# Performance work log

Measured on AMD Instinct MI355X. Metric: run time of the kernel, lower is better.

## Reference

```python
import jax, jax.numpy as jnp
import numpy as np

N, F, H, O = 3072, 128, 16, 8  # nodes, in_channels, hidden_channels, out_channels


def setup_inputs() -> dict:
    key = jax.random.key(0)
    ks = jax.random.split(key, 8)
    s = 0.01  # xavier gain=0.01 in original init -> small weights
    return {
        "x": jax.random.normal(ks[0], (N, F), dtype=jnp.float32),
        "edge_index": jax.random.randint(ks[1], (2, N * 32), 0, N, dtype=jnp.int64),
        "node_distances": jax.random.uniform(ks[2], (N, N), dtype=jnp.float32),
        "normalization_matrix": jnp.ones((N, N), dtype=jnp.float32),
        # per-feature MLPs fs[f]: Linear(1,H) -> ReLU -> (Dropout p=0) -> Linear(H,O), stacked over F
        "W1": s * jax.random.normal(ks[3], (F, H), dtype=jnp.float32),
        "b1": jnp.zeros((F, H), dtype=jnp.float32),
        "W2": s * jax.random.normal(ks[4], (F, H, O), dtype=jnp.float32),
        "b2": jnp.zeros((F, O), dtype=jnp.float32),
        # rho MLP: Linear(1,H) -> ReLU -> Linear(H,O) (bias=True since is_graph_task=False)
        "rW1": s * jax.random.normal(ks[5], (H,), dtype=jnp.float32),
        "rb1": jnp.zeros((H,), dtype=jnp.float32),
        "rW2": s * jax.random.normal(ks[6], (H, O), dtype=jnp.float32),
        "rb2": jnp.zeros((O,), dtype=jnp.float32),
    }


def reference(x, edge_index, node_distances, normalization_matrix,
              W1, b1, W2, b2, rW1, rb1, rW2, rb2):
    # --- per-feature tiny MLPs, vectorized over the feature axis ---
    # h[n,f,:] = relu(x[n,f] * W1[f] + b1[f])
    h = jax.nn.relu(x[:, :, None] * W1[None, :, :] + b1[None, :, :])  # [N,F,H]
    fx = jnp.einsum('nfh,fho->nfo', h, W2) + b2[None, :, :]           # [N,F,O]
    # sum over features first (commutes with the matmul's F-reduction)
    g = fx.sum(axis=1)                                                 # [N,O]

    # --- rho MLP on normalized pairwise distances ---
    d = node_distances / normalization_matrix                          # [N,N]
    hd = jax.nn.relu(d[:, :, None] * rW1 + rb1)                        # [N,N,H]
    m = jnp.einsum('nmh,ho->nmo', hd, rW2) + rb2                       # [N,N,O]

    # out.T in torch: mf = m_dist_perm @ fx_perm summed over features -> [N,O]
    out = jnp.einsum('nmo,mo->no', m, g)                               # [N,O]
    return out
```

## Files before the change

kernel.cpp:

```cpp
#include <hip/hip_runtime.h>
#include <hip/hip_bf16.h>
#include <math.h>

#define NN 3072
#define FF 128
#define HH 16
#define OO 8

#define MC   1024
#define NCH  3
#define RPB  8

#define OFF_GT   0

#define NPB 4

__global__ __launch_bounds__(128) void gnan_g_kernel(
    const float* __restrict__ x,
    const float* __restrict__ W1,
    const float* __restrict__ b1,
    const float* __restrict__ W2,
    const float* __restrict__ b2,
    float* __restrict__ gT,
    float* __restrict__ out)
{
    const int f  = threadIdx.x;
    const int n0 = blockIdx.x * NPB;

    {
        const int gid = blockIdx.x * 128 + threadIdx.x;
        if (gid < NN * OO / 4)
            reinterpret_cast<float4*>(out)[gid] = make_float4(0.f, 0.f, 0.f, 0.f);
    }

    float xv[NPB];
#pragma unroll
    for (int ni = 0; ni < NPB; ++ni)
        xv[ni] = x[(size_t)(n0 + ni) * FF + f];

    const float4 b2a = *reinterpret_cast<const float4*>(b2 + f * OO);
    const float4 b2b = *reinterpret_cast<const float4*>(b2 + f * OO + 4);

    float acc[NPB][OO];
#pragma unroll
    for (int ni = 0; ni < NPB; ++ni) {
        acc[ni][0] = b2a.x; acc[ni][1] = b2a.y; acc[ni][2] = b2a.z; acc[ni][3] = b2a.w;
        acc[ni][4] = b2b.x; acc[ni][5] = b2b.y; acc[ni][6] = b2b.z; acc[ni][7] = b2b.w;
    }

    for (int h = 0; h < HH; ++h) {
        const float w1h = W1[f * HH + h];
        const float b1h = b1[f * HH + h];
        const float4 wa = *reinterpret_cast<const float4*>(W2 + (size_t)(f * HH + h) * OO);
        const float4 wb = *reinterpret_cast<const float4*>(W2 + (size_t)(f * HH + h) * OO + 4);
#pragma unroll
        for (int ni = 0; ni < NPB; ++ni) {
            const float a = fmaxf(fmaf(xv[ni], w1h, b1h), 0.f);
            acc[ni][0] = fmaf(a, wa.x, acc[ni][0]);
            acc[ni][1] = fmaf(a, wa.y, acc[ni][1]);
            acc[ni][2] = fmaf(a, wa.z, acc[ni][2]);
            acc[ni][3] = fmaf(a, wa.w, acc[ni][3]);
            acc[ni][4] = fmaf(a, wb.x, acc[ni][4]);
            acc[ni][5] = fmaf(a, wb.y, acc[ni][5]);
            acc[ni][6] = fmaf(a, wb.z, acc[ni][6]);
            acc[ni][7] = fmaf(a, wb.w, acc[ni][7]);
        }
    }

    __shared__ float wsum[NPB][2][OO];
    const int lane = threadIdx.x & 63;
    const int wid  = threadIdx.x >> 6;
#pragma unroll
    for (int ni = 0; ni < NPB; ++ni) {
#pragma unroll
        for (int o = 0; o < OO; ++o) {
#pragma unroll
            for (int off = 32; off > 0; off >>= 1)
                acc[ni][o] += __shfl_down(acc[ni][o], off);
        }
        if (lane == 0) {
#pragma unroll
            for (int o = 0; o < OO; ++o) wsum[ni][wid][o] = acc[ni][o];
        }
    }
    __syncthreads();
    if (threadIdx.x < NPB * OO) {
        const int ni = threadIdx.x >> 3, o = threadIdx.x & 7;
        gT[o * NN + (n0 + ni)] = wsum[ni][0][o] + wsum[ni][1][o];
    }
}

__device__ __forceinline__ void accum_one(
    float d, float clo, float chi, const float gk[OO],
    float dg[OO], float corr[OO],
    const float* KpS, const float (*rowsS)[16], const float* refB)
{
    if (d >= clo && d < chi) {
#pragma unroll
        for (int o = 0; o < OO; ++o) dg[o] = fmaf(d, gk[o], dg[o]);
    } else {
        int j = 0;
#pragma unroll
        for (int p = 0; p < HH; ++p) j += (d >= KpS[1 + p]) ? 1 : 0;
#pragma unroll
        for (int o = 0; o < OO; ++o) {
            const float v = fmaf(rowsS[j][o], d, rowsS[j][8 + o]) - refB[o];
            corr[o] = fmaf(v, gk[o], corr[o]);
        }
    }
}

__global__ __launch_bounds__(512) void gnan_main_kernel(
    const float* __restrict__ nd,
    const float* __restrict__ nm,
    const float* __restrict__ wsf,
    const float* __restrict__ rW1,
    const float* __restrict__ rb1,
    const float* __restrict__ rW2,
    const float* __restrict__ rb2,
    float* __restrict__ out)
{
    __shared__ float gs[OO * MC];
    __shared__ float gsum[OO];
    __shared__ float KpS[HH + 2];
    __shared__ float rowsS[HH + 1][16];
    __shared__ float refS[18];

    const int t  = threadIdx.x;
    const int b  = blockIdx.x;
    const int rg = b / NCH;
    const int c  = b % NCH;

    {
        float4*       dst = reinterpret_cast<float4*>(gs);
        const float4* src = reinterpret_cast<const float4*>(wsf + OFF_GT);
#pragma unroll
        for (int r = 0; r < OO * MC / 4 / 512; ++r) {
            const int i  = r * 512 + t;
            const int o  = i >> 8;
            const int mi = i & 255;
            dst[i] = src[o * (NN / 4) + c * (MC / 4) + mi];
        }
    }

    if (t < (HH + 1) * OO + 2) {
        float w[HH], bb[HH], knee[HH];
#pragma unroll
        for (int h = 0; h < HH; ++h) {
            w[h]  = rW1[h];
            bb[h] = rb1[h];
            knee[h] = (w[h] != 0.f) ? (-bb[h] / w[h]) : INFINITY;
        }
        if (t >= (HH + 1) * OO) {
            KpS[(t - (HH + 1) * OO) * (HH + 1)] =
                (t == (HH + 1) * OO) ? -INFINITY : INFINITY;
        } else {
            const int j = t >> 3, o = t & 7;
            if (o == 0 && j < HH) {
                int r = 0;
#pragma unroll
                for (int h2 = 0; h2 < HH; ++h2)
                    r += (knee[h2] < knee[j] || (knee[h2] == knee[j] && h2 < j)) ? 1 : 0;
                KpS[1 + r] = knee[j];
            }
            float cAdd = rb2[o];
#pragma unroll
            for (int h = 0; h < HH; ++h)
                if (w[h] == 0.f) cAdd += fmaxf(bb[h], 0.f) * rW2[h * OO + o];

            float alpha = 0.f, beta = 0.f;
#pragma unroll
            for (int h = 0; h < HH; ++h) {
                int r = 0;
#pragma unroll
                for (int h2 = 0; h2 < HH; ++h2)
                    r += (knee[h2] < knee[h] || (knee[h2] == knee[h] && h2 < h)) ? 1 : 0;
                const bool active = (w[h] > 0.f) ? (r < j)
                                  : (w[h] < 0.f ? (r >= j) : false);
                if (active) {
                    alpha += w[h]  * rW2[h * OO + o];
                    beta  += bb[h] * rW2[h * OO + o];
                }
            }
            const float betaF = beta + cAdd;
            rowsS[j][o]     = alpha;
            rowsS[j][8 + o] = betaF;

            const float d00 = nd[0] / nm[0];
            int j0 = 0;
#pragma unroll
            for (int h = 0; h < HH; ++h) j0 += (d00 >= knee[h]) ? 1 : 0;
            if (j == j0) {
                refS[2 + o]  = alpha;
                refS[10 + o] = betaF;
                if (o == 0) {
                    float clo = -INFINITY, chi = INFINITY;
#pragma unroll
                    for (int h = 0; h < HH; ++h) {
                        if (d00 >= knee[h]) clo = fmaxf(clo, knee[h]);
                        else                chi = fminf(chi, knee[h]);
                    }
                    refS[0] = clo;
                    refS[1] = chi;
                }
            }
        }
    }
    __syncthreads();

    const int wave = t >> 6;
    const int lane = t & 63;

    {
        float s = 0.f;
        for (int i = lane; i < MC; i += 64) s += gs[wave * MC + i];
#pragma unroll
        for (int off = 32; off > 0; off >>= 1) s += __shfl_down(s, off);
        if (lane == 0) gsum[wave] = s;
    }

    const float clo = refS[0];
    const float chi = refS[1];
    const float* refB = &refS[10];

    const int row = rg * RPB + wave;
    const float* __restrict__ drow = nd + (size_t)row * NN + c * MC;
    const float* __restrict__ nrow = nm + (size_t)row * NN + c * MC;

    float dg[OO], corr[OO];
#pragma unroll
    for (int o = 0; o < OO; ++o) { dg[o] = 0.f; corr[o] = 0.f; }

    for (int it = 0; it < MC / 256; ++it) {
        const int m0 = it * 256 + lane * 4;
        const float4 dv = *reinterpret_cast<const float4*>(drow + m0);
        const float4 nv = *reinterpret_cast<const float4*>(nrow + m0);
        float4 gv[OO];
#pragma unroll
        for (int o = 0; o < OO; ++o)
            gv[o] = *reinterpret_cast<const float4*>(&gs[o * MC + m0]);

        {
            float gk[OO];
#pragma unroll
            for (int o = 0; o < OO; ++o) gk[o] = gv[o].x;
            accum_one(__fdividef(dv.x, nv.x), clo, chi, gk, dg, corr, KpS, rowsS, refB);
        }
        {
            float gk[OO];
#pragma unroll
            for (int o = 0; o < OO; ++o) gk[o] = gv[o].y;
            accum_one(__fdividef(dv.y, nv.y), clo, chi, gk, dg, corr, KpS, rowsS, refB);
        }
        {
            float gk[OO];
#pragma unroll
            for (int o = 0; o < OO; ++o) gk[o] = gv[o].z;
            accum_one(__fdividef(dv.z, nv.z), clo, chi, gk, dg, corr, KpS, rowsS, refB);
        }
        {
            float gk[OO];
#pragma unroll
            for (int o = 0; o < OO; ++o) gk[o] = gv[o].w;
            accum_one(__fdividef(dv.w, nv.w), clo, chi, gk, dg, corr, KpS, rowsS, refB);
        }
    }

    float val[OO];
#pragma unroll
    for (int o = 0; o < OO; ++o)
        val[o] = fmaf(refS[2 + o], dg[o], corr[o]);
#pragma unroll
    for (int o = 0; o < OO; ++o) {
#pragma unroll
        for (int off = 32; off > 0; off >>= 1)
            val[o] += __shfl_down(val[o], off);
    }
    if (lane == 0) {
#pragma unroll
        for (int o = 0; o < OO; ++o)
            atomicAdd(out + (size_t)row * OO + o,
                      fmaf(refB[o], gsum[o], val[o]));
    }
}

extern "C" void kernel_launch(void* const* d_in, const int* in_sizes, int n_in,
                              void* d_out, int out_size, void* d_ws, size_t ws_size,
                              hipStream_t stream) {
    const float* x   = (const float*)d_in[0];
    const float* nd  = (const float*)d_in[2];
    const float* nm  = (const float*)d_in[3];
    const float* W1  = (const float*)d_in[4];
    const float* b1  = (const float*)d_in[5];
    const float* W2  = (const float*)d_in[6];
    const float* b2  = (const float*)d_in[7];
    const float* rW1 = (const float*)d_in[8];
    const float* rb1 = (const float*)d_in[9];
    const float* rW2 = (const float*)d_in[10];
    const float* rb2 = (const float*)d_in[11];
    float* out = (float*)d_out;
    float* wsf = (float*)d_ws;

    gnan_g_kernel<<<NN / NPB, 128, 0, stream>>>(x, W1, b1, W2, b2,
                                                wsf + OFF_GT, out);
    gnan_main_kernel<<<(NN / RPB) * NCH, 512, 0, stream>>>(
        nd, nm, wsf, rW1, rb1, rW2, rb2, out);
}
```

Before: 167.9 us.

## Process full rows per wave, read g from global, drop atomics and LDS staging

The main kernel now assigns one full row of the distance matrix to each wave (4 rows per 256-thread block) instead of splitting rows into three column chunks across blocks. g is read straight from global/L2 rather than staged in shared memory, and the per-row g sum is accumulated in registers alongside the main loop. Each output is then written with a plain store, so the zeroing pass in the first kernel and the atomicAdds go away. The trade-off is fewer blocks (768 vs 1152), more global g traffic per wave, and extra adds per element.

```diff
diff --git a/kernel.cpp b/kernel.cpp
--- a/kernel.cpp
+++ b/kernel.cpp
@@ -6,10 +6,6 @@
 #define FF 128
 #define HH 16
 #define OO 8
-
-#define MC   1024
-#define NCH  3
-#define RPB  8
 
 #define OFF_GT   0
 
@@ -21,17 +17,10 @@
     const float* __restrict__ b1,
     const float* __restrict__ W2,
     const float* __restrict__ b2,
-    float* __restrict__ gT,
-    float* __restrict__ out)
+    float* __restrict__ gT)
 {
     const int f  = threadIdx.x;
     const int n0 = blockIdx.x * NPB;
-
-    {
-        const int gid = blockIdx.x * 128 + threadIdx.x;
-        if (gid < NN * OO / 4)
-            reinterpret_cast<float4*>(out)[gid] = make_float4(0.f, 0.f, 0.f, 0.f);
-    }
 
     float xv[NPB];
 #pragma unroll
@@ -92,9 +81,11 @@
 
 __device__ __forceinline__ void accum_one(
     float d, float clo, float chi, const float gk[OO],
-    float dg[OO], float corr[OO],
+    float dg[OO], float sg[OO], float corr[OO],
     const float* KpS, const float (*rowsS)[16], const float* refB)
 {
+#pragma unroll
+    for (int o = 0; o < OO; ++o) sg[o] += gk[o];
     if (d >= clo && d < chi) {
 #pragma unroll
         for (int o = 0; o < OO; ++o) dg[o] = fmaf(d, gk[o], dg[o]);
@@ -110,38 +101,21 @@
     }
 }
 
-__global__ __launch_bounds__(512) void gnan_main_kernel(
+__global__ __launch_bounds__(256) void gnan_main_kernel(
     const float* __restrict__ nd,
     const float* __restrict__ nm,
-    const float* __restrict__ wsf,
+    const float* __restrict__ gT,
     const float* __restrict__ rW1,
     const float* __restrict__ rb1,
     const float* __restrict__ rW2,
     const float* __restrict__ rb2,
     float* __restrict__ out)
 {
-    __shared__ float gs[OO * MC];
-    __shared__ float gsum[OO];
     __shared__ float KpS[HH + 2];
     __shared__ float rowsS[HH + 1][16];
     __shared__ float refS[18];
 
-    const int t  = threadIdx.x;
-    const int b  = blockIdx.x;
-    const int rg = b / NCH;
-    const int c  = b % NCH;
-
-    {
-        float4*       dst = reinterpret_cast<float4*>(gs);
-        const float4* src = reinterpret_cast<const float4*>(wsf + OFF_GT);
-#pragma unroll
-        for (int r = 0; r < OO * MC / 4 / 512; ++r) {
-            const int i  = r * 512 + t;
-            const int o  = i >> 8;
-            const int mi = i & 255;
-            dst[i] = src[o * (NN / 4) + c * (MC / 4) + mi];
-        }
-    }
+    const int t = threadIdx.x;
 
     if (t < (HH + 1) * OO + 2) {
         float w[HH], bb[HH], knee[HH];
@@ -210,66 +184,58 @@
 
     const int wave = t >> 6;
     const int lane = t & 63;
-
-    {
-        float s = 0.f;
-        for (int i = lane; i < MC; i += 64) s += gs[wave * MC + i];
-#pragma unroll
-        for (int off = 32; off > 0; off >>= 1) s += __shfl_down(s, off);
-        if (lane == 0) gsum[wave] = s;
-    }
+    const int row  = blockIdx.x * 4 + wave;
 
     const float clo = refS[0];
     const float chi = refS[1];
     const float* refB = &refS[10];
 
-    const int row = rg * RPB + wave;
-    const float* __restrict__ drow = nd + (size_t)row * NN + c * MC;
-    const float* __restrict__ nrow = nm + (size_t)row * NN + c * MC;
-
-    float dg[OO], corr[OO];
-#pragma unroll
-    for (int o = 0; o < OO; ++o) { dg[o] = 0.f; corr[o] = 0.f; }
-
-    for (int it = 0; it < MC / 256; ++it) {
+    const float* __restrict__ drow = nd + (size_t)row * NN;
+    const float* __restrict__ nrow = nm + (size_t)row * NN;
+
+    float dg[OO], sg[OO], corr[OO];
+#pragma unroll
+    for (int o = 0; o < OO; ++o) { dg[o] = 0.f; sg[o] = 0.f; corr[o] = 0.f; }
+
+    for (int it = 0; it < NN / 256; ++it) {
         const int m0 = it * 256 + lane * 4;
         const float4 dv = *reinterpret_cast<const float4*>(drow + m0);
         const float4 nv = *reinterpret_cast<const float4*>(nrow + m0);
         float4 gv[OO];
 #pragma unroll
         for (int o = 0; o < OO; ++o)
-            gv[o] = *reinterpret_cast<const float4*>(&gs[o * MC + m0]);
+            gv[o] = *reinterpret_cast<const float4*>(&gT[o * NN + m0]);
 
         {
             float gk[OO];
 #pragma unroll
             for (int o = 0; o < OO; ++o) gk[o] = gv[o].x;
-            accum_one(__fdividef(dv.x, nv.x), clo, chi, gk, dg, corr, KpS, rowsS, refB);
+            accum_one(__fdividef(dv.x, nv.x), clo, chi, gk, dg, sg, corr, KpS, rowsS, refB);
         }
         {
             float gk[OO];
 #pragma unroll
             for (int o = 0; o < OO; ++o) gk[o] = gv[o].y;
-            accum_one(__fdividef(dv.y, nv.y), clo, chi, gk, dg, corr, KpS, rowsS, refB);
+            accum_one(__fdividef(dv.y, nv.y), clo, chi, gk, dg, sg, corr, KpS, rowsS, refB);
         }
         {
             float gk[OO];
 #pragma unroll
             for (int o = 0; o < OO; ++o) gk[o] = gv[o].z;
-            accum_one(__fdividef(dv.z, nv.z), clo, chi, gk, dg, corr, KpS, rowsS, refB);
+            accum_one(__fdividef(dv.z, nv.z), clo, chi, gk, dg, sg, corr, KpS, rowsS, refB);
         }
         {
             float gk[OO];
 #pragma unroll
             for (int o = 0; o < OO; ++o) gk[o] = gv[o].w;
-            accum_one(__fdividef(dv.w, nv.w), clo, chi, gk, dg, corr, KpS, rowsS, refB);
+            accum_one(__fdividef(dv.w, nv.w), clo, chi, gk, dg, sg, corr, KpS, rowsS, refB);
         }
     }
 
     float val[OO];
 #pragma unroll
     for (int o = 0; o < OO; ++o)
-        val[o] = fmaf(refS[2 + o], dg[o], corr[o]);
+        val[o] = fmaf(refS[2 + o], dg[o], fmaf(refB[o], sg[o], corr[o]));
 #pragma unroll
     for (int o = 0; o < OO; ++o) {
 #pragma unroll
@@ -279,8 +245,7 @@
     if (lane == 0) {
 #pragma unroll
         for (int o = 0; o < OO; ++o)
-            atomicAdd(out + (size_t)row * OO + o,
-                      fmaf(refB[o], gsum[o], val[o]));
+            out[(size_t)row * OO + o] = val[o];
     }
 }
 
@@ -301,8 +266,7 @@
     float* out = (float*)d_out;
     float* wsf = (float*)d_ws;
 
-    gnan_g_kernel<<<NN / NPB, 128, 0, stream>>>(x, W1, b1, W2, b2,
-                                                wsf + OFF_GT, out);
-    gnan_main_kernel<<<(NN / RPB) * NCH, 512, 0, stream>>>(
-        nd, nm, wsf, rW1, rb1, rW2, rb2, out);
-}
+    gnan_g_kernel<<<NN / NPB, 128, 0, stream>>>(x, W1, b1, W2, b2, wsf + OFF_GT);
+    gnan_main_kernel<<<NN / 4, 256, 0, stream>>>(
+        nd, nm, wsf + OFF_GT, rW1, rb1, rW2, rb2, out);
+}
```

New measurement: 163.4 us. 1.03x faster.
